# Kernel optimization log

Measured on AMD Instinct MI355X. Metric: run time of the kernel, lower is better.

Reference implementation:

```python
import jax, jax.numpy as jnp
import numpy as np

B, D, H, W = 1, 16, 16, 16
C, NH = 528, 8
HD = C // NH      # 66
K = 32            # retrieved memories per token


def setup_inputs() -> dict:
    key = jax.random.key(0)
    ks = jax.random.split(key, 4)
    x = jax.random.normal(ks[0], (B, D, H, W, C), jnp.float32)
    # simulated knn_memory.search output: (B, heads, N, K, 2[k/v], head_dim)
    knn_kv = jax.random.normal(ks[1], (B, NH, D * H * W, K, 2, HD), jnp.float32)
    w_qkv = jax.random.normal(ks[2], (3 * C, C), jnp.float32) * 0.02
    b_qkv = jnp.zeros((3 * C,), jnp.float32)
    w_proj = jax.random.normal(ks[3], (C, C), jnp.float32) * 0.02
    b_proj = jnp.zeros((C,), jnp.float32)
    return {"x": x, "knn_kv": knn_kv, "w_qkv": w_qkv, "b_qkv": b_qkv,
            "w_proj": w_proj, "b_proj": b_proj, "num_heads": NH}


def _l2norm(t):
    # F.normalize(t, dim=-1): t / max(||t||_2, eps)
    n = jnp.linalg.norm(t, axis=-1, keepdims=True)
    return t / jnp.maximum(n, 1e-12)


def _forward(x, knn_kv, w_qkv, b_qkv, w_proj, b_proj, num_heads):
    Bb, Dd, Hh, Ww, Cc = x.shape
    N = Dd * Hh * Ww
    hd = Cc // num_heads
    scaling = hd ** -0.5
    qkv = x.reshape(Bb * N, Cc) @ w_qkv.T + b_qkv
    qkv = qkv.reshape(Bb, N, 3, num_heads, hd).transpose(2, 0, 3, 1, 4)  # (3,B,h,N,hd)
    q, k, v = qkv[0], qkv[1], qkv[2]
    q = _l2norm(q)
    k = _l2norm(k)
    knn_k = knn_kv[..., 0, :]   # (B,h,N,K,hd)
    knn_v = knn_kv[..., 1, :]
    k_comb = jnp.concatenate([knn_k, k[..., None, :]], axis=-2)  # (B,h,N,K+1,hd)
    v_comb = jnp.concatenate([knn_v, v[..., None, :]], axis=-2)
    attn = jnp.einsum('bhnd,bhnkd->bhnk', q, k_comb) * scaling
    attn = jax.nn.softmax(attn, axis=-1)  # stable softmax
    out = jnp.einsum('bhnk,bhnkd->bhnd', attn, v_comb)  # (B,h,N,hd)
    out = out.transpose(0, 2, 1, 3).reshape(Bb * N, num_heads * hd)
    out = out @ w_proj.T + b_proj
    return out.reshape(Bb, Dd, Hh, Ww, Cc)


def reference(x, knn_kv, w_qkv, b_qkv, w_proj, b_proj, num_heads):
    return _forward(x, knn_kv, w_qkv, b_qkv, w_proj, b_proj, num_heads)
```

## Files before the change

### kernel.cpp

```cpp
#include <hip/hip_runtime.h>
#include <hip/hip_bf16.h>
#include <math.h>

#define N_POS 4096
#define C_DIM 528
#define NHEAD 8
#define HDIM  66
#define KNN   32
#define CQKV  1584
#define KP    544
#define NP1   1664
#define NP2   640

typedef __attribute__((ext_vector_type(8))) short short8;
typedef __attribute__((ext_vector_type(4))) float f32x4;
typedef __hip_bfloat16 bf16;

typedef const __attribute__((address_space(1))) void* gas1;
typedef __attribute__((address_space(3))) void* las3;

__global__ __launch_bounds__(256) void convpad3_kernel(
    const float* __restrict__ x, const float* __restrict__ wq,
    const float* __restrict__ wp,
    bf16* __restrict__ xb, bf16* __restrict__ wqb, bf16* __restrict__ wpb)
{
    int b = blockIdx.x;
    const float* src; bf16* dst; int Nr;
    if (b < N_POS)            { src = x;  dst = xb;  Nr = N_POS; }
    else if (b < N_POS + NP1) { b -= N_POS; src = wq; dst = wqb; Nr = CQKV; }
    else                      { b -= N_POS + NP1; src = wp; dst = wpb; Nr = C_DIM; }
    for (int c = threadIdx.x; c < KP; c += 256) {
        float v = (b < Nr && c < C_DIM) ? src[(size_t)b * C_DIM + c] : 0.0f;
        dst[(size_t)b * KP + c] = __float2bfloat16(v);
    }
}

template <bool BF16OUT>
__global__ __launch_bounds__(256) void gemm_mfma_kernel(
    const bf16* __restrict__ A, const bf16* __restrict__ B,
    const float* __restrict__ bias, void* __restrict__ Cv,
    int Nreal, int ldc, int nbx)
{
    __shared__ bf16 As[2][64 * 32];
    __shared__ bf16 Bs[2][64 * 32];

    const int tid  = threadIdx.x;
    const int lane = tid & 63;
    const int wid  = tid >> 6;

    const int nwg   = gridDim.x;
    const int chunk = nwg >> 3;
    const int swz   = (blockIdx.x & 7) * chunk + (blockIdx.x >> 3);
    const int bm = (swz / nbx) * 64;
    const int bn = (swz % nbx) * 64;

    const int r   = (wid << 4) + (lane >> 2);
    const int csw = ((lane & 3) ^ ((r >> 1) & 3)) << 3;

    const bf16* Ag = A + (size_t)(bm + r) * KP + csw;
    const bf16* Bg = B + (size_t)(bn + r) * KP + csw;

    bf16* as0 = &As[0][0] + (wid << 4) * 32;
    bf16* bs0 = &Bs[0][0] + (wid << 4) * 32;
    const int BUF = 64 * 32;

    const int wm = (wid >> 1) * 32;
    const int wn = (wid & 1) * 32;
    const int arow = wm + (lane & 15);
    const int brow = wn + (lane & 15);
    const int seg  = lane >> 4;
    const int aoff = (seg ^ ((arow >> 1) & 3)) << 3;
    const int boff = (seg ^ ((brow >> 1) & 3)) << 3;

    f32x4 acc[2][2];
    #pragma unroll
    for (int i = 0; i < 2; ++i)
        #pragma unroll
        for (int j = 0; j < 2; ++j)
            acc[i][j] = (f32x4){0.f, 0.f, 0.f, 0.f};

    __builtin_amdgcn_global_load_lds((gas1)(Ag), (las3)(as0), 16, 0, 0);
    __builtin_amdgcn_global_load_lds((gas1)(Bg), (las3)(bs0), 16, 0, 0);
    __syncthreads();

    int cur = 0;
    for (int k0 = 0; k0 < KP; k0 += 32) {
        if (k0 + 32 < KP) {
            const int nb = cur ^ 1;
            __builtin_amdgcn_global_load_lds((gas1)(Ag + k0 + 32), (las3)(as0 + nb * BUF), 16, 0, 0);
            __builtin_amdgcn_global_load_lds((gas1)(Bg + k0 + 32), (las3)(bs0 + nb * BUF), 16, 0, 0);
        }

        const bf16* ab = &As[cur][0];
        const bf16* bb = &Bs[cur][0];
        short8 af[2], bfr[2];
        #pragma unroll
        for (int f = 0; f < 2; ++f)
            af[f] = *(const short8*)&ab[(arow + f * 16) * 32 + aoff];
        #pragma unroll
        for (int f = 0; f < 2; ++f)
            bfr[f] = *(const short8*)&bb[(brow + f * 16) * 32 + boff];

        #pragma unroll
        for (int i = 0; i < 2; ++i)
            #pragma unroll
            for (int j = 0; j < 2; ++j)
                acc[i][j] = __builtin_amdgcn_mfma_f32_16x16x32_bf16(
                    af[i], bfr[j], acc[i][j], 0, 0, 0);

        __syncthreads();
        cur ^= 1;
    }

    #pragma unroll
    for (int i = 0; i < 2; ++i) {
        const int row = bm + wm + i * 16 + (lane >> 4) * 4;
        #pragma unroll
        for (int j = 0; j < 2; ++j) {
            const int col = bn + wn + j * 16 + (lane & 15);
            if (col < Nreal) {
                const float bv = bias[col];
                #pragma unroll
                for (int rr = 0; rr < 4; ++rr) {
                    const float o = acc[i][j][rr] + bv;
                    if (BF16OUT)
                        ((bf16*)Cv)[(size_t)(row + rr) * ldc + col] = __float2bfloat16(o);
                    else
                        ((float*)Cv)[(size_t)(row + rr) * ldc + col] = o;
                }
            }
        }
    }
}

__global__ __launch_bounds__(256) void attn_kernel(
    const bf16* __restrict__ qkv, const float* __restrict__ knn,
    bf16* __restrict__ out)
{
    const float scaling = 0.12309149097933272f;

    const int bid = blockIdx.x;
    const int tid = threadIdx.x;
    const int g0  = bid << 1;
    const int h   = g0 >> 12;
    const int n0  = g0 & 4095;
    const int n1  = n0 + 1;

    __shared__ float s_knn[2][KNN * 132];
    __shared__ float s_qkv[2][3 * HDIM];
    __shared__ float s_dot[2][KNN + 1];
    __shared__ float s_sc[2][2];

    const float4* kb0 = (const float4*)(knn + (size_t)g0 * (KNN * 132));
    const float4* kb1 = kb0 + KNN * 33;
    float4 r0[4], r1[4];
    float4 e0 = {0.f, 0.f, 0.f, 0.f}, e1 = {0.f, 0.f, 0.f, 0.f};
    #pragma unroll
    for (int i = 0; i < 4; ++i) r0[i] = kb0[tid + 256 * i];
    if (tid < 32) e0 = kb0[1024 + tid];
    #pragma unroll
    for (int i = 0; i < 4; ++i) r1[i] = kb1[tid + 256 * i];
    if (tid < 32) e1 = kb1[1024 + tid];

    const bf16* qp0 = qkv + (size_t)n0 * CQKV + h * HDIM;
    const bf16* qp1 = qp0 + CQKV;
    float qv0 = 0.f, qv1 = 0.f;
    int part = tid / HDIM, d66 = tid - part * HDIM;
    if (tid < 3 * HDIM) {
        qv0 = __bfloat162float(qp0[part * C_DIM + d66]);
        qv1 = __bfloat162float(qp1[part * C_DIM + d66]);
    }

    float4* s40 = (float4*)s_knn[0];
    float4* s41 = (float4*)s_knn[1];
    #pragma unroll
    for (int i = 0; i < 4; ++i) s40[tid + 256 * i] = r0[i];
    if (tid < 32) s40[1024 + tid] = e0;
    #pragma unroll
    for (int i = 0; i < 4; ++i) s41[tid + 256 * i] = r1[i];
    if (tid < 32) s41[1024 + tid] = e1;
    if (tid < 3 * HDIM) {
        s_qkv[0][tid] = qv0;
        s_qkv[1][tid] = qv1;
    }
    __syncthreads();

    const int team  = tid >> 7;
    const int ttid  = tid & 127;
    const int twave = ttid >> 6;
    const int lane  = tid & 63;
    const float* kK = s_knn[team];
    const float* Q  = &s_qkv[team][0];
    const float* KS = &s_qkv[team][HDIM];

    if (twave == 0) {
        const int j = lane >> 1, l2 = lane & 1;
        const float* kr = kK + j * 132;
        float p = 0.f;
        #pragma unroll
        for (int d = 0; d < HDIM / 2; ++d) p += Q[2 * d + l2] * kr[2 * d + l2];
        p += __shfl_xor(p, 1);
        if (l2 == 0) s_dot[team][j] = p;
    } else {
        float aq, ak, qk;
        {
            float qd = Q[lane], kd = KS[lane];
            aq = qd * qd; ak = kd * kd; qk = qd * kd;
            if (lane < 2) {
                float q2 = Q[64 + lane], k2 = KS[64 + lane];
                aq += q2 * q2; ak += k2 * k2; qk += q2 * k2;
            }
        }
        #pragma unroll
        for (int off = 32; off; off >>= 1) {
            aq += __shfl_xor(aq, off);
            ak += __shfl_xor(ak, off);
            qk += __shfl_xor(qk, off);
        }
        if (lane == 0) {
            const float iq = 1.0f / fmaxf(sqrtf(aq), 1e-12f);
            const float ik = 1.0f / fmaxf(sqrtf(ak), 1e-12f);
            s_sc[team][0] = iq * scaling;
            s_sc[team][1] = qk * iq * ik * scaling;
        }
    }
    __syncthreads();

    if (twave == 0) {
        float x = -3.4e38f;
        if (lane < 32)       x = s_dot[team][lane] * s_sc[team][0];
        else if (lane == 32) x = s_sc[team][1];
        float m = x;
        #pragma unroll
        for (int off = 32; off; off >>= 1) m = fmaxf(m, __shfl_xor(m, off));
        float e = (lane < 33) ? expf(x - m) : 0.f;
        float s = e;
        #pragma unroll
        for (int off = 32; off; off >>= 1) s += __shfl_xor(s, off);
        if (lane < 33) s_dot[team][lane] = e / s;
    }
    __syncthreads();

    if (ttid < HDIM) {
        const int d = ttid;
        float acc = s_dot[team][KNN] * s_qkv[team][2 * HDIM + d];
        #pragma unroll 8
        for (int j = 0; j < KNN; ++j)
            acc += s_dot[team][j] * kK[j * 132 + HDIM + d];
        const int n = team ? n1 : n0;
        out[(size_t)n * KP + h * HDIM + d] = __float2bfloat16(acc);
    }
    if (h == 0) {
        if (tid < 16)
            out[(size_t)n0 * KP + C_DIM + tid] = __float2bfloat16(0.f);
        else if (tid < 32)
            out[(size_t)n1 * KP + C_DIM + (tid - 16)] = __float2bfloat16(0.f);
    }
}

extern "C" void kernel_launch(void* const* d_in, const int* in_sizes, int n_in,
                              void* d_out, int out_size, void* d_ws, size_t ws_size,
                              hipStream_t stream)
{
    const float* x      = (const float*)d_in[0];
    const float* knn_kv = (const float*)d_in[1];
    const float* w_qkv  = (const float*)d_in[2];
    const float* b_qkv  = (const float*)d_in[3];
    const float* w_proj = (const float*)d_in[4];
    const float* b_proj = (const float*)d_in[5];
    float* out = (float*)d_out;

    char* ws = (char*)d_ws;
    bf16* qkvb = (bf16*)ws;
    bf16* xb   = (bf16*)(ws + 12976128);
    bf16* wqb  = (bf16*)(ws + 12976128 + 4456448);
    bf16* wpb  = (bf16*)(ws + 12976128 + 4456448 + 1810432);
    bf16* ab   = (bf16*)(ws + 12976128 + 4456448 + 1810432 + 696320);

    convpad3_kernel<<<N_POS + NP1 + NP2, 256, 0, stream>>>(x, w_qkv, w_proj, xb, wqb, wpb);

    gemm_mfma_kernel<true><<<dim3((NP1 / 64) * (N_POS / 64)), 256, 0, stream>>>(
        xb, wqb, b_qkv, qkvb, CQKV, CQKV, NP1 / 64);

    attn_kernel<<<dim3(NHEAD * N_POS / 2), 256, 0, stream>>>(qkvb, knn_kv, ab);

    gemm_mfma_kernel<false><<<dim3((NP2 / 64) * (N_POS / 64)), 256, 0, stream>>>(
        ab, wpb, b_proj, out, C_DIM, C_DIM, NP2 / 64);
}
```

Baseline: 171.8 us.

## Make attention kernel persistent with register-prefetched next tile

After: 293.0 us. +70.6%, slower.

```diff
diff --git a/kernel.cpp b/kernel.cpp
--- a/kernel.cpp
+++ b/kernel.cpp
@@ -11,6 +11,9 @@
 #define KP    544
 #define NP1   1664
 #define NP2   640
+
+#define ATTN_BLOCKS 1024
+#define ATTN_ITERS  16
 
 typedef __attribute__((ext_vector_type(8))) short short8;
 typedef __attribute__((ext_vector_type(4))) float f32x4;
@@ -135,126 +138,176 @@
 
 __global__ __launch_bounds__(256) void attn_kernel(
     const bf16* __restrict__ qkv, const float* __restrict__ knn,
-    bf16* __restrict__ out)
+    bf16* __restrict__ out, int iters)
 {
     const float scaling = 0.12309149097933272f;
 
-    const int bid = blockIdx.x;
     const int tid = threadIdx.x;
-    const int g0  = bid << 1;
-    const int h   = g0 >> 12;
-    const int n0  = g0 & 4095;
-    const int n1  = n0 + 1;
 
     __shared__ float s_knn[2][KNN * 132];
     __shared__ float s_qkv[2][3 * HDIM];
     __shared__ float s_dot[2][KNN + 1];
     __shared__ float s_sc[2][2];
 
-    const float4* kb0 = (const float4*)(knn + (size_t)g0 * (KNN * 132));
-    const float4* kb1 = kb0 + KNN * 33;
-    float4 r0[4], r1[4];
-    float4 e0 = {0.f, 0.f, 0.f, 0.f}, e1 = {0.f, 0.f, 0.f, 0.f};
-    #pragma unroll
-    for (int i = 0; i < 4; ++i) r0[i] = kb0[tid + 256 * i];
-    if (tid < 32) e0 = kb0[1024 + tid];
-    #pragma unroll
-    for (int i = 0; i < 4; ++i) r1[i] = kb1[tid + 256 * i];
-    if (tid < 32) e1 = kb1[1024 + tid];
-
-    const bf16* qp0 = qkv + (size_t)n0 * CQKV + h * HDIM;
-    const bf16* qp1 = qp0 + CQKV;
-    float qv0 = 0.f, qv1 = 0.f;
-    int part = tid / HDIM, d66 = tid - part * HDIM;
-    if (tid < 3 * HDIM) {
-        qv0 = __bfloat162float(qp0[part * C_DIM + d66]);
-        qv1 = __bfloat162float(qp1[part * C_DIM + d66]);
-    }
-
-    float4* s40 = (float4*)s_knn[0];
-    float4* s41 = (float4*)s_knn[1];
-    #pragma unroll
-    for (int i = 0; i < 4; ++i) s40[tid + 256 * i] = r0[i];
-    if (tid < 32) s40[1024 + tid] = e0;
-    #pragma unroll
-    for (int i = 0; i < 4; ++i) s41[tid + 256 * i] = r1[i];
-    if (tid < 32) s41[1024 + tid] = e1;
-    if (tid < 3 * HDIM) {
-        s_qkv[0][tid] = qv0;
-        s_qkv[1][tid] = qv1;
+    const int part = tid / HDIM;
+    const int d66  = tid - part * HDIM;
+
+    int it = blockIdx.x * iters;
+
+    {
+        const int g0 = it << 1;
+        const float4* kb0 = (const float4*)(knn + (size_t)g0 * (KNN * 132));
+        const float4* kb1 = kb0 + KNN * 33;
+        float4 r0[4], r1[4];
+        float4 e0 = {0.f,0.f,0.f,0.f}, e1 = {0.f,0.f,0.f,0.f};
+        #pragma unroll
+        for (int i = 0; i < 4; ++i) r0[i] = kb0[tid + 256 * i];
+        if (tid < 32) e0 = kb0[1024 + tid];
+        #pragma unroll
+        for (int i = 0; i < 4; ++i) r1[i] = kb1[tid + 256 * i];
+        if (tid < 32) e1 = kb1[1024 + tid];
+
+        const int h0 = g0 >> 12, n0 = g0 & 4095;
+        const bf16* qp0 = qkv + (size_t)n0 * CQKV + h0 * HDIM;
+        const bf16* qp1 = qp0 + CQKV;
+        float qv0 = 0.f, qv1 = 0.f;
+        if (tid < 3 * HDIM) {
+            qv0 = __bfloat162float(qp0[part * C_DIM + d66]);
+            qv1 = __bfloat162float(qp1[part * C_DIM + d66]);
+        }
+
+        float4* s40 = (float4*)s_knn[0];
+        float4* s41 = (float4*)s_knn[1];
+        #pragma unroll
+        for (int i = 0; i < 4; ++i) s40[tid + 256 * i] = r0[i];
+        if (tid < 32) s40[1024 + tid] = e0;
+        #pragma unroll
+        for (int i = 0; i < 4; ++i) s41[tid + 256 * i] = r1[i];
+        if (tid < 32) s41[1024 + tid] = e1;
+        if (tid < 3 * HDIM) {
+            s_qkv[0][tid] = qv0;
+            s_qkv[1][tid] = qv1;
+        }
     }
     __syncthreads();
 
-    const int team  = tid >> 7;
-    const int ttid  = tid & 127;
-    const int twave = ttid >> 6;
-    const int lane  = tid & 63;
-    const float* kK = s_knn[team];
-    const float* Q  = &s_qkv[team][0];
-    const float* KS = &s_qkv[team][HDIM];
-
-    if (twave == 0) {
-        const int j = lane >> 1, l2 = lane & 1;
-        const float* kr = kK + j * 132;
-        float p = 0.f;
-        #pragma unroll
-        for (int d = 0; d < HDIM / 2; ++d) p += Q[2 * d + l2] * kr[2 * d + l2];
-        p += __shfl_xor(p, 1);
-        if (l2 == 0) s_dot[team][j] = p;
-    } else {
-        float aq, ak, qk;
-        {
-            float qd = Q[lane], kd = KS[lane];
-            aq = qd * qd; ak = kd * kd; qk = qd * kd;
-            if (lane < 2) {
-                float q2 = Q[64 + lane], k2 = KS[64 + lane];
-                aq += q2 * q2; ak += k2 * k2; qk += q2 * k2;
-            }
-        }
-        #pragma unroll
-        for (int off = 32; off; off >>= 1) {
-            aq += __shfl_xor(aq, off);
-            ak += __shfl_xor(ak, off);
-            qk += __shfl_xor(qk, off);
-        }
-        if (lane == 0) {
-            const float iq = 1.0f / fmaxf(sqrtf(aq), 1e-12f);
-            const float ik = 1.0f / fmaxf(sqrtf(ak), 1e-12f);
-            s_sc[team][0] = iq * scaling;
-            s_sc[team][1] = qk * iq * ik * scaling;
-        }
-    }
-    __syncthreads();
-
-    if (twave == 0) {
-        float x = -3.4e38f;
-        if (lane < 32)       x = s_dot[team][lane] * s_sc[team][0];
-        else if (lane == 32) x = s_sc[team][1];
-        float m = x;
-        #pragma unroll
-        for (int off = 32; off; off >>= 1) m = fmaxf(m, __shfl_xor(m, off));
-        float e = (lane < 33) ? expf(x - m) : 0.f;
-        float s = e;
-        #pragma unroll
-        for (int off = 32; off; off >>= 1) s += __shfl_xor(s, off);
-        if (lane < 33) s_dot[team][lane] = e / s;
-    }
-    __syncthreads();
-
-    if (ttid < HDIM) {
-        const int d = ttid;
-        float acc = s_dot[team][KNN] * s_qkv[team][2 * HDIM + d];
-        #pragma unroll 8
-        for (int j = 0; j < KNN; ++j)
-            acc += s_dot[team][j] * kK[j * 132 + HDIM + d];
-        const int n = team ? n1 : n0;
-        out[(size_t)n * KP + h * HDIM + d] = __float2bfloat16(acc);
-    }
-    if (h == 0) {
-        if (tid < 16)
-            out[(size_t)n0 * KP + C_DIM + tid] = __float2bfloat16(0.f);
-        else if (tid < 32)
-            out[(size_t)n1 * KP + C_DIM + (tid - 16)] = __float2bfloat16(0.f);
+    for (int t = 0; t < iters; ++t, ++it) {
+        const bool hasNext = (t + 1 < iters);
+        float4 r0[4], r1[4];
+        float4 e0 = {0.f,0.f,0.f,0.f}, e1 = {0.f,0.f,0.f,0.f};
+        float qv0 = 0.f, qv1 = 0.f;
+        if (hasNext) {
+            const int gn = (it + 1) << 1;
+            const float4* kb0 = (const float4*)(knn + (size_t)gn * (KNN * 132));
+            const float4* kb1 = kb0 + KNN * 33;
+            #pragma unroll
+            for (int i = 0; i < 4; ++i) r0[i] = kb0[tid + 256 * i];
+            if (tid < 32) e0 = kb0[1024 + tid];
+            #pragma unroll
+            for (int i = 0; i < 4; ++i) r1[i] = kb1[tid + 256 * i];
+            if (tid < 32) e1 = kb1[1024 + tid];
+            const int hn = gn >> 12, nn = gn & 4095;
+            const bf16* qp0 = qkv + (size_t)nn * CQKV + hn * HDIM;
+            const bf16* qp1 = qp0 + CQKV;
+            if (tid < 3 * HDIM) {
+                qv0 = __bfloat162float(qp0[part * C_DIM + d66]);
+                qv1 = __bfloat162float(qp1[part * C_DIM + d66]);
+            }
+        }
+
+        const int g0 = it << 1;
+        const int h  = g0 >> 12;
+        const int n0 = g0 & 4095;
+        const int n1 = n0 + 1;
+
+        const int team  = tid >> 7;
+        const int ttid  = tid & 127;
+        const int twave = ttid >> 6;
+        const int lane  = tid & 63;
+        const float* kK = s_knn[team];
+        const float* Q  = &s_qkv[team][0];
+        const float* KS = &s_qkv[team][HDIM];
+
+        if (twave == 0) {
+            const int j = lane >> 1, l2 = lane & 1;
+            const float* kr = kK + j * 132;
+            float p = 0.f;
+            #pragma unroll
+            for (int d = 0; d < HDIM / 2; ++d) p += Q[2 * d + l2] * kr[2 * d + l2];
+            p += __shfl_xor(p, 1);
+            if (l2 == 0) s_dot[team][j] = p;
+        } else {
+            float aq, ak, qk;
+            {
+                float qd = Q[lane], kd = KS[lane];
+                aq = qd * qd; ak = kd * kd; qk = qd * kd;
+                if (lane < 2) {
+                    float q2 = Q[64 + lane], k2 = KS[64 + lane];
+                    aq += q2 * q2; ak += k2 * k2; qk += q2 * k2;
+                }
+            }
+            #pragma unroll
+            for (int off = 32; off; off >>= 1) {
+                aq += __shfl_xor(aq, off);
+                ak += __shfl_xor(ak, off);
+                qk += __shfl_xor(qk, off);
+            }
+            if (lane == 0) {
+                const float iq = 1.0f / fmaxf(sqrtf(aq), 1e-12f);
+                const float ik = 1.0f / fmaxf(sqrtf(ak), 1e-12f);
+                s_sc[team][0] = iq * scaling;
+                s_sc[team][1] = qk * iq * ik * scaling;
+            }
+        }
+        __syncthreads();
+
+        if (twave == 0) {
+            float x = -3.4e38f;
+            if (lane < 32)       x = s_dot[team][lane] * s_sc[team][0];
+            else if (lane == 32) x = s_sc[team][1];
+            float m = x;
+            #pragma unroll
+            for (int off = 32; off; off >>= 1) m = fmaxf(m, __shfl_xor(m, off));
+            float e = (lane < 33) ? expf(x - m) : 0.f;
+            float s = e;
+            #pragma unroll
+            for (int off = 32; off; off >>= 1) s += __shfl_xor(s, off);
+            if (lane < 33) s_dot[team][lane] = e / s;
+        }
+        __syncthreads();
+
+        if (ttid < HDIM) {
+            const int d = ttid;
+            float acc = s_dot[team][KNN] * s_qkv[team][2 * HDIM + d];
+            #pragma unroll 8
+            for (int j = 0; j < KNN; ++j)
+                acc += s_dot[team][j] * kK[j * 132 + HDIM + d];
+            const int n = team ? n1 : n0;
+            out[(size_t)n * KP + h * HDIM + d] = __float2bfloat16(acc);
+        }
+        if (h == 0) {
+            if (tid < 16)
+                out[(size_t)n0 * KP + C_DIM + tid] = __float2bfloat16(0.f);
+            else if (tid < 32)
+                out[(size_t)n1 * KP + C_DIM + (tid - 16)] = __float2bfloat16(0.f);
+        }
+
+        __syncthreads();
+        if (hasNext) {
+            float4* s40 = (float4*)s_knn[0];
+            float4* s41 = (float4*)s_knn[1];
+            #pragma unroll
+            for (int i = 0; i < 4; ++i) s40[tid + 256 * i] = r0[i];
+            if (tid < 32) s40[1024 + tid] = e0;
+            #pragma unroll
+            for (int i = 0; i < 4; ++i) s41[tid + 256 * i] = r1[i];
+            if (tid < 32) s41[1024 + tid] = e1;
+            if (tid < 3 * HDIM) {
+                s_qkv[0][tid] = qv0;
+                s_qkv[1][tid] = qv1;
+            }
+        }
+        __syncthreads();
     }
 }
 
@@ -282,7 +335,7 @@
     gemm_mfma_kernel<true><<<dim3((NP1 / 64) * (N_POS / 64)), 256, 0, stream>>>(
         xb, wqb, b_qkv, qkvb, CQKV, CQKV, NP1 / 64);
 
-    attn_kernel<<<dim3(NHEAD * N_POS / 2), 256, 0, stream>>>(qkvb, knn_kv, ab);
+    attn_kernel<<<dim3(ATTN_BLOCKS), 256, 0, stream>>>(qkvb, knn_kv, ab, ATTN_ITERS);
 
     gemm_mfma_kernel<false><<<dim3((NP2 / 64) * (N_POS / 64)), 256, 0, stream>>>(
         ab, wpb, b_proj, out, C_DIM, C_DIM, NP2 / 64);
```

## Make attention kernel persistent with double-buffered async global-to-LDS staging

Applied to the files above, without the earlier changes.

Result: slower. 177.7 us (+3.5%).

```diff
diff --git a/kernel.cpp b/kernel.cpp
--- a/kernel.cpp
+++ b/kernel.cpp
@@ -11,6 +11,9 @@
 #define KP    544
 #define NP1   1664
 #define NP2   640
+
+#define ATTN_BLOCKS 1024
+#define ATTN_ITERS  16
 
 typedef __attribute__((ext_vector_type(8))) short short8;
 typedef __attribute__((ext_vector_type(4))) float f32x4;
@@ -135,127 +138,143 @@
 
 __global__ __launch_bounds__(256) void attn_kernel(
     const bf16* __restrict__ qkv, const float* __restrict__ knn,
-    bf16* __restrict__ out)
+    bf16* __restrict__ out, int iters)
 {
     const float scaling = 0.12309149097933272f;
 
-    const int bid = blockIdx.x;
-    const int tid = threadIdx.x;
-    const int g0  = bid << 1;
-    const int h   = g0 >> 12;
-    const int n0  = g0 & 4095;
-    const int n1  = n0 + 1;
-
-    __shared__ float s_knn[2][KNN * 132];
-    __shared__ float s_qkv[2][3 * HDIM];
+    const int tid  = threadIdx.x;
+    const int wid  = tid >> 6;
+    const int lane = tid & 63;
+    const int part = tid / HDIM;
+    const int d66  = tid - part * HDIM;
+
+    __shared__ float s_knn[2][2 * KNN * 132];
+    __shared__ float s_qkv[2][2][3 * HDIM];
     __shared__ float s_dot[2][KNN + 1];
     __shared__ float s_sc[2][2];
 
-    const float4* kb0 = (const float4*)(knn + (size_t)g0 * (KNN * 132));
-    const float4* kb1 = kb0 + KNN * 33;
-    float4 r0[4], r1[4];
-    float4 e0 = {0.f, 0.f, 0.f, 0.f}, e1 = {0.f, 0.f, 0.f, 0.f};
-    #pragma unroll
-    for (int i = 0; i < 4; ++i) r0[i] = kb0[tid + 256 * i];
-    if (tid < 32) e0 = kb0[1024 + tid];
-    #pragma unroll
-    for (int i = 0; i < 4; ++i) r1[i] = kb1[tid + 256 * i];
-    if (tid < 32) e1 = kb1[1024 + tid];
-
-    const bf16* qp0 = qkv + (size_t)n0 * CQKV + h * HDIM;
-    const bf16* qp1 = qp0 + CQKV;
-    float qv0 = 0.f, qv1 = 0.f;
-    int part = tid / HDIM, d66 = tid - part * HDIM;
-    if (tid < 3 * HDIM) {
-        qv0 = __bfloat162float(qp0[part * C_DIM + d66]);
-        qv1 = __bfloat162float(qp1[part * C_DIM + d66]);
+    int it = blockIdx.x * iters;
+
+    #define STAGE_KNN(buf, group0)                                               \
+        do {                                                                     \
+            const char* _src = (const char*)(knn + (size_t)(group0) * (KNN * 132)); \
+            char* _dst = (char*)&s_knn[buf][0];                                  \
+            _Pragma("unroll")                                                    \
+            for (int _i = 0; _i < 8; ++_i) {                                     \
+                const int _s = wid * 8 + _i;                                     \
+                __builtin_amdgcn_global_load_lds(                                \
+                    (gas1)(_src + _s * 1024 + lane * 16),                        \
+                    (las3)(_dst + _s * 1024), 16, 0, 0);                         \
+            }                                                                    \
+            if (wid == 3)                                                        \
+                __builtin_amdgcn_global_load_lds(                                \
+                    (gas1)(_src + 32 * 1024 + lane * 16),                        \
+                    (las3)(_dst + 32 * 1024), 16, 0, 0);                         \
+        } while (0)
+
+    #define STAGE_QKV(buf, group0)                                               \
+        do {                                                                     \
+            if (tid < 3 * HDIM) {                                                \
+                const int _n0 = (group0) & 4095, _h = (group0) >> 12;            \
+                const bf16* _qp = qkv + (size_t)_n0 * CQKV + _h * HDIM;          \
+                s_qkv[buf][0][tid] = __bfloat162float(_qp[part * C_DIM + d66]);  \
+                s_qkv[buf][1][tid] = __bfloat162float(_qp[CQKV + part * C_DIM + d66]); \
+            }                                                                    \
+        } while (0)
+
+    STAGE_KNN(0, it << 1);
+    STAGE_QKV(0, it << 1);
+    __syncthreads();
+
+    int cur = 0;
+    for (int t = 0; t < iters; ++t, ++it) {
+        const int nb = cur ^ 1;
+        if (t + 1 < iters) {
+            STAGE_KNN(nb, (it + 1) << 1);
+            STAGE_QKV(nb, (it + 1) << 1);
+        }
+
+        const int g0 = it << 1;
+        const int h  = g0 >> 12;
+        const int n0 = g0 & 4095;
+        const int n1 = n0 + 1;
+
+        const int team  = tid >> 7;
+        const int ttid  = tid & 127;
+        const int twave = ttid >> 6;
+        const float* kK = &s_knn[cur][team * (KNN * 132)];
+        const float* Q  = &s_qkv[cur][team][0];
+        const float* KS = &s_qkv[cur][team][HDIM];
+
+        if (twave == 0) {
+            const int j = lane >> 1, l2 = lane & 1;
+            const float* kr = kK + j * 132;
+            float p = 0.f;
+            #pragma unroll
+            for (int d = 0; d < HDIM / 2; ++d) p += Q[2 * d + l2] * kr[2 * d + l2];
+            p += __shfl_xor(p, 1);
+            if (l2 == 0) s_dot[team][j] = p;
+        } else {
+            float aq, ak, qk;
+            {
+                float qd = Q[lane], kd = KS[lane];
+                aq = qd * qd; ak = kd * kd; qk = qd * kd;
+                if (lane < 2) {
+                    float q2 = Q[64 + lane], k2 = KS[64 + lane];
+                    aq += q2 * q2; ak += k2 * k2; qk += q2 * k2;
+                }
+            }
+            #pragma unroll
+            for (int off = 32; off; off >>= 1) {
+                aq += __shfl_xor(aq, off);
+                ak += __shfl_xor(ak, off);
+                qk += __shfl_xor(qk, off);
+            }
+            if (lane == 0) {
+                const float iq = 1.0f / fmaxf(sqrtf(aq), 1e-12f);
+                const float ik = 1.0f / fmaxf(sqrtf(ak), 1e-12f);
+                s_sc[team][0] = iq * scaling;
+                s_sc[team][1] = qk * iq * ik * scaling;
+            }
+        }
+        __syncthreads();
+
+        if (twave == 0) {
+            float x = -3.4e38f;
+            if (lane < 32)       x = s_dot[team][lane] * s_sc[team][0];
+            else if (lane == 32) x = s_sc[team][1];
+            float m = x;
+            #pragma unroll
+            for (int off = 32; off; off >>= 1) m = fmaxf(m, __shfl_xor(m, off));
+            float e = (lane < 33) ? expf(x - m) : 0.f;
+            float s = e;
+            #pragma unroll
+            for (int off = 32; off; off >>= 1) s += __shfl_xor(s, off);
+            if (lane < 33) s_dot[team][lane] = e / s;
+        }
+        __syncthreads();
+
+        if (ttid < HDIM) {
+            const int d = ttid;
+            float acc = s_dot[team][KNN] * s_qkv[cur][team][2 * HDIM + d];
+            #pragma unroll 8
+            for (int j = 0; j < KNN; ++j)
+                acc += s_dot[team][j] * kK[j * 132 + HDIM + d];
+            const int n = team ? n1 : n0;
+            out[(size_t)n * KP + h * HDIM + d] = __float2bfloat16(acc);
+        }
+        if (h == 0) {
+            if (tid < 16)
+                out[(size_t)n0 * KP + C_DIM + tid] = __float2bfloat16(0.f);
+            else if (tid < 32)
+                out[(size_t)n1 * KP + C_DIM + (tid - 16)] = __float2bfloat16(0.f);
+        }
+
+        __syncthreads();
+        cur = nb;
     }
-
-    float4* s40 = (float4*)s_knn[0];
-    float4* s41 = (float4*)s_knn[1];
-    #pragma unroll
-    for (int i = 0; i < 4; ++i) s40[tid + 256 * i] = r0[i];
-    if (tid < 32) s40[1024 + tid] = e0;
-    #pragma unroll
-    for (int i = 0; i < 4; ++i) s41[tid + 256 * i] = r1[i];
-    if (tid < 32) s41[1024 + tid] = e1;
-    if (tid < 3 * HDIM) {
-        s_qkv[0][tid] = qv0;
-        s_qkv[1][tid] = qv1;
-    }
-    __syncthreads();
-
-    const int team  = tid >> 7;
-    const int ttid  = tid & 127;
-    const int twave = ttid >> 6;
-    const int lane  = tid & 63;
-    const float* kK = s_knn[team];
-    const float* Q  = &s_qkv[team][0];
-    const float* KS = &s_qkv[team][HDIM];
-
-    if (twave == 0) {
-        const int j = lane >> 1, l2 = lane & 1;
-        const float* kr = kK + j * 132;
-        float p = 0.f;
-        #pragma unroll
-        for (int d = 0; d < HDIM / 2; ++d) p += Q[2 * d + l2] * kr[2 * d + l2];
-        p += __shfl_xor(p, 1);
-        if (l2 == 0) s_dot[team][j] = p;
-    } else {
-        float aq, ak, qk;
-        {
-            float qd = Q[lane], kd = KS[lane];
-            aq = qd * qd; ak = kd * kd; qk = qd * kd;
-            if (lane < 2) {
-                float q2 = Q[64 + lane], k2 = KS[64 + lane];
-                aq += q2 * q2; ak += k2 * k2; qk += q2 * k2;
-            }
-        }
-        #pragma unroll
-        for (int off = 32; off; off >>= 1) {
-            aq += __shfl_xor(aq, off);
-            ak += __shfl_xor(ak, off);
-            qk += __shfl_xor(qk, off);
-        }
-        if (lane == 0) {
-            const float iq = 1.0f / fmaxf(sqrtf(aq), 1e-12f);
-            const float ik = 1.0f / fmaxf(sqrtf(ak), 1e-12f);
-            s_sc[team][0] = iq * scaling;
-            s_sc[team][1] = qk * iq * ik * scaling;
-        }
-    }
-    __syncthreads();
-
-    if (twave == 0) {
-        float x = -3.4e38f;
-        if (lane < 32)       x = s_dot[team][lane] * s_sc[team][0];
-        else if (lane == 32) x = s_sc[team][1];
-        float m = x;
-        #pragma unroll
-        for (int off = 32; off; off >>= 1) m = fmaxf(m, __shfl_xor(m, off));
-        float e = (lane < 33) ? expf(x - m) : 0.f;
-        float s = e;
-        #pragma unroll
-        for (int off = 32; off; off >>= 1) s += __shfl_xor(s, off);
-        if (lane < 33) s_dot[team][lane] = e / s;
-    }
-    __syncthreads();
-
-    if (ttid < HDIM) {
-        const int d = ttid;
-        float acc = s_dot[team][KNN] * s_qkv[team][2 * HDIM + d];
-        #pragma unroll 8
-        for (int j = 0; j < KNN; ++j)
-            acc += s_dot[team][j] * kK[j * 132 + HDIM + d];
-        const int n = team ? n1 : n0;
-        out[(size_t)n * KP + h * HDIM + d] = __float2bfloat16(acc);
-    }
-    if (h == 0) {
-        if (tid < 16)
-            out[(size_t)n0 * KP + C_DIM + tid] = __float2bfloat16(0.f);
-        else if (tid < 32)
-            out[(size_t)n1 * KP + C_DIM + (tid - 16)] = __float2bfloat16(0.f);
-    }
+    #undef STAGE_KNN
+    #undef STAGE_QKV
 }
 
 extern "C" void kernel_launch(void* const* d_in, const int* in_sizes, int n_in,
@@ -282,7 +301,7 @@
     gemm_mfma_kernel<true><<<dim3((NP1 / 64) * (N_POS / 64)), 256, 0, stream>>>(
         xb, wqb, b_qkv, qkvb, CQKV, CQKV, NP1 / 64);
 
-    attn_kernel<<<dim3(NHEAD * N_POS / 2), 256, 0, stream>>>(qkvb, knn_kv, ab);
+    attn_kernel<<<dim3(ATTN_BLOCKS), 256, 0, stream>>>(qkvb, knn_kv, ab, ATTN_ITERS);
 
     gemm_mfma_kernel<false><<<dim3((NP2 / 64) * (N_POS / 64)), 256, 0, stream>>>(
         ab, wpb, b_proj, out, C_DIM, C_DIM, NP2 / 64);
```

## Fuse fp32-to-bf16 conversion into GEMM loads and drop separate convert kernel

Applied to the files above, without the earlier changes.

Result: no change. 173.8 us (+1.2%).

```diff
diff --git a/kernel.cpp b/kernel.cpp
--- a/kernel.cpp
+++ b/kernel.cpp
@@ -16,33 +16,28 @@
 typedef __attribute__((ext_vector_type(4))) float f32x4;
 typedef __hip_bfloat16 bf16;
 
-typedef const __attribute__((address_space(1))) void* gas1;
-typedef __attribute__((address_space(3))) void* las3;
-
-__global__ __launch_bounds__(256) void convpad3_kernel(
-    const float* __restrict__ x, const float* __restrict__ wq,
-    const float* __restrict__ wp,
-    bf16* __restrict__ xb, bf16* __restrict__ wqb, bf16* __restrict__ wpb)
-{
-    int b = blockIdx.x;
-    const float* src; bf16* dst; int Nr;
-    if (b < N_POS)            { src = x;  dst = xb;  Nr = N_POS; }
-    else if (b < N_POS + NP1) { b -= N_POS; src = wq; dst = wqb; Nr = CQKV; }
-    else                      { b -= N_POS + NP1; src = wp; dst = wpb; Nr = C_DIM; }
-    for (int c = threadIdx.x; c < KP; c += 256) {
-        float v = (b < Nr && c < C_DIM) ? src[(size_t)b * C_DIM + c] : 0.0f;
-        dst[(size_t)b * KP + c] = __float2bfloat16(v);
-    }
-}
-
-template <bool BF16OUT>
-__global__ __launch_bounds__(256) void gemm_mfma_kernel(
-    const bf16* __restrict__ A, const bf16* __restrict__ B,
+__device__ __forceinline__ short bf16bits(float f) {
+    bf16 h = __float2bfloat16(f);
+    return *reinterpret_cast<short*>(&h);
+}
+__device__ __forceinline__ short8 pack8(float4 a, float4 b) {
+    short8 r;
+    r[0] = bf16bits(a.x); r[1] = bf16bits(a.y);
+    r[2] = bf16bits(a.z); r[3] = bf16bits(a.w);
+    r[4] = bf16bits(b.x); r[5] = bf16bits(b.y);
+    r[6] = bf16bits(b.z); r[7] = bf16bits(b.w);
+    return r;
+}
+
+template <bool A_F32, bool BF16OUT>
+__global__ __launch_bounds__(256) void gemm_fused_kernel(
+    const void* __restrict__ Av, int lda,
+    const float* __restrict__ B, int Brows,
     const float* __restrict__ bias, void* __restrict__ Cv,
     int Nreal, int ldc, int nbx)
 {
-    __shared__ bf16 As[2][64 * 32];
-    __shared__ bf16 Bs[2][64 * 32];
+    __shared__ short8 As[256];
+    __shared__ short8 Bs[256];
 
     const int tid  = threadIdx.x;
     const int lane = tid & 63;
@@ -54,23 +49,44 @@
     const int bm = (swz / nbx) * 64;
     const int bn = (swz % nbx) * 64;
 
-    const int r   = (wid << 4) + (lane >> 2);
-    const int csw = ((lane & 3) ^ ((r >> 1) & 3)) << 3;
-
-    const bf16* Ag = A + (size_t)(bm + r) * KP + csw;
-    const bf16* Bg = B + (size_t)(bn + r) * KP + csw;
-
-    bf16* as0 = &As[0][0] + (wid << 4) * 32;
-    bf16* bs0 = &Bs[0][0] + (wid << 4) * 32;
-    const int BUF = 64 * 32;
+    const int r0 = tid >> 2;
+    const int c0 = tid & 3;
+    const int w0 = r0 * 4 + (c0 ^ (r0 & 3));
+    const bool bRowOk = (bn + r0) < Brows;
 
     const int wm = (wid >> 1) * 32;
     const int wn = (wid & 1) * 32;
     const int arow = wm + (lane & 15);
     const int brow = wn + (lane & 15);
-    const int seg  = lane >> 4;
-    const int aoff = (seg ^ ((arow >> 1) & 3)) << 3;
-    const int boff = (seg ^ ((brow >> 1) & 3)) << 3;
+    const int apc  = lane >> 4;
+    const int aslot = arow * 4 + (apc ^ (arow & 3));
+    const int bslot = brow * 4 + (apc ^ (brow & 3));
+
+    auto loadA = [&](int k0) -> short8 {
+        const int c = k0 + c0 * 8;
+        if constexpr (A_F32) {
+            float4 f0 = {0.f,0.f,0.f,0.f}, f1 = {0.f,0.f,0.f,0.f};
+            if (c <= C_DIM - 8) {
+                const float* ap = (const float*)Av + (size_t)(bm + r0) * lda + c;
+                f0 = *(const float4*)ap;
+                f1 = *(const float4*)(ap + 4);
+            }
+            return pack8(f0, f1);
+        } else {
+            const bf16* ap = (const bf16*)Av + (size_t)(bm + r0) * lda + c;
+            return *(const short8*)ap;
+        }
+    };
+    auto loadB = [&](int k0) -> short8 {
+        const int c = k0 + c0 * 8;
+        float4 f0 = {0.f,0.f,0.f,0.f}, f1 = {0.f,0.f,0.f,0.f};
+        if (c <= C_DIM - 8 && bRowOk) {
+            const float* bp = B + (size_t)(bn + r0) * C_DIM + c;
+            f0 = *(const float4*)bp;
+            f1 = *(const float4*)(bp + 4);
+        }
+        return pack8(f0, f1);
+    };
 
     f32x4 acc[2][2];
     #pragma unroll
@@ -79,37 +95,30 @@
         for (int j = 0; j < 2; ++j)
             acc[i][j] = (f32x4){0.f, 0.f, 0.f, 0.f};
 
-    __builtin_amdgcn_global_load_lds((gas1)(Ag), (las3)(as0), 16, 0, 0);
-    __builtin_amdgcn_global_load_lds((gas1)(Bg), (las3)(bs0), 16, 0, 0);
-    __syncthreads();
-
-    int cur = 0;
-    for (int k0 = 0; k0 < KP; k0 += 32) {
+    short8 a0 = loadA(0);
+    short8 b0 = loadB(0);
+
+    for (int k0 = 0;; k0 += 32) {
+        As[w0] = a0;
+        Bs[w0] = b0;
+        __syncthreads();
         if (k0 + 32 < KP) {
-            const int nb = cur ^ 1;
-            __builtin_amdgcn_global_load_lds((gas1)(Ag + k0 + 32), (las3)(as0 + nb * BUF), 16, 0, 0);
-            __builtin_amdgcn_global_load_lds((gas1)(Bg + k0 + 32), (las3)(bs0 + nb * BUF), 16, 0, 0);
-        }
-
-        const bf16* ab = &As[cur][0];
-        const bf16* bb = &Bs[cur][0];
+            a0 = loadA(k0 + 32);
+            b0 = loadB(k0 + 32);
+        }
         short8 af[2], bfr[2];
         #pragma unroll
-        for (int f = 0; f < 2; ++f)
-            af[f] = *(const short8*)&ab[(arow + f * 16) * 32 + aoff];
-        #pragma unroll
-        for (int f = 0; f < 2; ++f)
-            bfr[f] = *(const short8*)&bb[(brow + f * 16) * 32 + boff];
-
+        for (int f = 0; f < 2; ++f) af[f]  = As[aslot + f * 64];
+        #pragma unroll
+        for (int f = 0; f < 2; ++f) bfr[f] = Bs[bslot + f * 64];
         #pragma unroll
         for (int i = 0; i < 2; ++i)
             #pragma unroll
             for (int j = 0; j < 2; ++j)
                 acc[i][j] = __builtin_amdgcn_mfma_f32_16x16x32_bf16(
                     af[i], bfr[j], acc[i][j], 0, 0, 0);
-
+        if (k0 + 32 >= KP) break;
         __syncthreads();
-        cur ^= 1;
     }
 
     #pragma unroll
@@ -154,7 +163,7 @@
     const float4* kb0 = (const float4*)(knn + (size_t)g0 * (KNN * 132));
     const float4* kb1 = kb0 + KNN * 33;
     float4 r0[4], r1[4];
-    float4 e0 = {0.f, 0.f, 0.f, 0.f}, e1 = {0.f, 0.f, 0.f, 0.f};
+    float4 e0 = {0.f,0.f,0.f,0.f}, e1 = {0.f,0.f,0.f,0.f};
     #pragma unroll
     for (int i = 0; i < 4; ++i) r0[i] = kb0[tid + 256 * i];
     if (tid < 32) e0 = kb0[1024 + tid];
@@ -272,18 +281,15 @@
 
     char* ws = (char*)d_ws;
     bf16* qkvb = (bf16*)ws;
-    bf16* xb   = (bf16*)(ws + 12976128);
-    bf16* wqb  = (bf16*)(ws + 12976128 + 4456448);
-    bf16* wpb  = (bf16*)(ws + 12976128 + 4456448 + 1810432);
-    bf16* ab   = (bf16*)(ws + 12976128 + 4456448 + 1810432 + 696320);
-
-    convpad3_kernel<<<N_POS + NP1 + NP2, 256, 0, stream>>>(x, w_qkv, w_proj, xb, wqb, wpb);
-
-    gemm_mfma_kernel<true><<<dim3((NP1 / 64) * (N_POS / 64)), 256, 0, stream>>>(
-        xb, wqb, b_qkv, qkvb, CQKV, CQKV, NP1 / 64);
+    bf16* ab   = (bf16*)(ws + 12976128);
+
+    gemm_fused_kernel<true, true>
+        <<<dim3((NP1 / 64) * (N_POS / 64)), 256, 0, stream>>>(
+        x, C_DIM, w_qkv, CQKV, b_qkv, qkvb, CQKV, CQKV, NP1 / 64);
 
     attn_kernel<<<dim3(NHEAD * N_POS / 2), 256, 0, stream>>>(qkvb, knn_kv, ab);
 
-    gemm_mfma_kernel<false><<<dim3((NP2 / 64) * (N_POS / 64)), 256, 0, stream>>>(
-        ab, wpb, b_proj, out, C_DIM, C_DIM, NP2 / 64);
-}
+    gemm_fused_kernel<false, false>
+        <<<dim3((NP2 / 64) * (N_POS / 64)), 256, 0, stream>>>(
+        ab, KP, w_proj, C_DIM, b_proj, out, C_DIM, C_DIM, NP2 / 64);
+}
```
